# Kernel optimization log

Measured on AMD Instinct MI355X. Metric: run time of the kernel, lower is better.

## Reference

```python
import jax, jax.numpy as jnp
import numpy as np

IN_DIM, OUT_DIM, NUM, K = 128, 128, 5, 3
SIZE = IN_DIM * OUT_DIM  # number of spline activations
BATCH = 1024


def extend_grid(grid, k):
    # pykan: pad grid by k uniform steps on each side -> (size, num+1+2k)
    h = (grid[:, -1:] - grid[:, :1]) / (grid.shape[1] - 1)
    for _ in range(k):
        grid = jnp.concatenate([grid[:, :1] - h, grid, grid[:, -1:] + h], axis=1)
    return grid


def b_batch(x, grid, k):
    # Cox-de-Boor recursion, unrolled over fixed order k.
    # x: (size, batch), grid: (size, P) already extended. Returns (size, P-1-k, batch).
    x = x[:, None, :]        # (size, 1, batch)
    g = grid[:, :, None]     # (size, P, 1)
    B = ((x >= g[:, :-1]) & (x < g[:, 1:])).astype(x.dtype)  # order 0
    for p in range(1, k + 1):
        B = (x - g[:, :-(p + 1)]) / (g[:, p:-1] - g[:, :-(p + 1)]) * B[:, :-1] \
          + (g[:, p + 1:] - x) / (g[:, p + 1:] - g[:, 1:-p]) * B[:, 1:]
    return B


def setup_inputs() -> dict:
    key = jax.random.key(0)
    k1, k2 = jax.random.split(key)
    x = jax.random.normal(k1, (BATCH, IN_DIM), dtype=jnp.float32)
    # grid: identical uniform rows, as in torch.einsum('i,j->ij', ones(size), linspace)
    grid = jnp.tile(jnp.linspace(-1.0, 1.0, NUM + 1, dtype=jnp.float32)[None, :], (SIZE, 1))
    # coef: (size, num+k) spline coefficients (stand-in for curve2coef init)
    coef = jax.random.normal(k2, (SIZE, NUM + K), dtype=jnp.float32) * 0.1
    scale_base = jnp.ones((SIZE,), jnp.float32)
    scale_sp = jnp.ones((SIZE,), jnp.float32)
    mask = jnp.ones((SIZE,), jnp.float32)
    return {"x": x, "grid": grid, "coef": coef,
            "scale_base": scale_base, "scale_sp": scale_sp, "mask": mask}


def reference(x, grid, coef, scale_base, scale_sp, mask):
    batch = x.shape[0]
    # fan out x over out_dim: einsum('ij,k->ikj').reshape(batch,size).T -> (size, batch)
    xe = jnp.broadcast_to(x[:, None, :], (batch, OUT_DIM, IN_DIM)).reshape(batch, SIZE).T
    preacts = xe.T.reshape(batch, OUT_DIM, IN_DIM)
    base = jax.nn.silu(xe).T                                   # (batch, size)
    B = b_batch(xe, extend_grid(grid, K), K)                   # (size, num+k, batch)
    spline = jnp.einsum('ij,ijk->ik', coef, B).T               # (batch, size)
    postspline = spline.reshape(batch, OUT_DIM, IN_DIM)
    y = mask[None, :] * (scale_base[None, :] * base + scale_sp[None, :] * spline)
    postacts = y.reshape(batch, OUT_DIM, IN_DIM)
    y_out = postacts.sum(axis=2)                               # (batch, out_dim)
    return y_out, preacts, postacts, postspline
```

## Files before the change

### kernel.cpp

```cpp
#include <hip/hip_runtime.h>


#define IN_DIM  128
#define OUT_DIM 128
#define NUMG    5
#define KORD    3
#define NB      8
#define SIZE    (IN_DIM * OUT_DIM)
#define BATCH   1024
#define G       8
#define JB      8
#define NBG     (BATCH / G)
#define NJO     (OUT_DIM / JB)

__global__ __launch_bounds__(256) void kan_fused(
    const float* __restrict__ x,
    const float* __restrict__ grid,
    const float* __restrict__ coef,
    const float* __restrict__ scale_base,
    const float* __restrict__ scale_sp,
    const float* __restrict__ mask,
    float* __restrict__ out)
{
    __shared__ float sBT[G][NB][IN_DIM];
    __shared__ float sSilu[G][IN_DIM];
    __shared__ float sXv[G][IN_DIM];

    const int tid = threadIdx.x;
    const int bg  = blockIdx.x >> 4;
    const int jo  = blockIdx.x & (NJO - 1);

    const int lane = tid & 63;
    const int w    = tid >> 6;
    const int il   = lane & 31;
    const int jh   = lane >> 5;
    const int i4   = il << 2;
    const int j    = jo * JB + w * 2 + jh;

    float4 cfq[8];
    {
        const float4* cp = (const float4*)coef;
        #pragma unroll
        for (int q = 0; q < 8; ++q)
            cfq[q] = cp[(size_t)j * 256 + il * 8 + q];
    }
    const int sS = j * IN_DIM + i4;
    const float4 mkv = *(const float4*)&mask[sS];
    const float4 sbv = *(const float4*)&scale_base[sS];
    const float4 ssv = *(const float4*)&scale_sp[sS];

    {
        const int i  = tid & 127;
        const int r0 = tid >> 7;

        float gr[NUMG + 1];
        #pragma unroll
        for (int rr = 0; rr <= NUMG; ++rr) gr[rr] = grid[i * (NUMG + 1) + rr];

        const float h = (gr[NUMG] - gr[0]) * (1.0f / NUMG);
        float t[NUMG + 1 + 2 * KORD];
        t[2] = gr[0] - h; t[1] = t[2] - h; t[0] = t[1] - h;
        #pragma unroll
        for (int rr = 0; rr <= NUMG; ++rr) t[KORD + rr] = gr[rr];
        t[9] = gr[NUMG] + h; t[10] = t[9] + h; t[11] = t[10] + h;

        float rcp1[11], rcp2[10], rcp3[9];
        #pragma unroll
        for (int m = 0; m < 11; ++m) rcp1[m] = 1.0f / (t[m + 1] - t[m]);
        #pragma unroll
        for (int m = 0; m < 10; ++m) rcp2[m] = 1.0f / (t[m + 2] - t[m]);
        #pragma unroll
        for (int m = 0; m < 9;  ++m) rcp3[m] = 1.0f / (t[m + 3] - t[m]);

        #pragma unroll
        for (int it = 0; it < 4; ++it) {
            const int r = it * 2 + r0;
            const float xv = x[(bg * G + r) * IN_DIM + i];

            float B[NUMG + 2 * KORD];
            #pragma unroll
            for (int m = 0; m < NUMG + 2 * KORD; ++m)
                B[m] = (xv >= t[m] && xv < t[m + 1]) ? 1.0f : 0.0f;
            #pragma unroll
            for (int m = 0; m < 10; ++m)
                B[m] = (xv - t[m]) * rcp1[m] * B[m]
                     + (t[m + 2] - xv) * rcp1[m + 1] * B[m + 1];
            #pragma unroll
            for (int m = 0; m < 9; ++m)
                B[m] = (xv - t[m]) * rcp2[m] * B[m]
                     + (t[m + 3] - xv) * rcp2[m + 1] * B[m + 1];
            #pragma unroll
            for (int m = 0; m < 8; ++m)
                B[m] = (xv - t[m]) * rcp3[m] * B[m]
                     + (t[m + 4] - xv) * rcp3[m + 1] * B[m + 1];

            #pragma unroll
            for (int m = 0; m < NB; ++m) sBT[r][m][i] = B[m];
            sSilu[r][i] = xv / (1.0f + __expf(-xv));
            sXv[r][i]   = xv;
        }
    }
    __syncthreads();

    float cfs[4][NB];
    #pragma unroll
    for (int k = 0; k < 4; ++k) {
        const float4 lo = cfq[2 * k], hi = cfq[2 * k + 1];
        cfs[k][0] = lo.x; cfs[k][1] = lo.y; cfs[k][2] = lo.z; cfs[k][3] = lo.w;
        cfs[k][4] = hi.x; cfs[k][5] = hi.y; cfs[k][6] = hi.z; cfs[k][7] = hi.w;
    }
    const float mkA[4] = {mkv.x, mkv.y, mkv.z, mkv.w};
    const float sbA[4] = {sbv.x, sbv.y, sbv.z, sbv.w};
    const float ssA[4] = {ssv.x, ssv.y, ssv.z, ssv.w};

    float* out_y   = out;
    float* out_pre = out + BATCH * OUT_DIM;
    float* out_act = out_pre + (size_t)BATCH * SIZE;
    float* out_spl = out_act + (size_t)BATCH * SIZE;

    float py[G];

    #pragma unroll
    for (int r = 0; r < G; ++r) {
        float4 bas[NB];
        #pragma unroll
        for (int m = 0; m < NB; ++m)
            bas[m] = *(const float4*)&sBT[r][m][i4];

        float sp0 = cfs[0][0] * bas[0].x;
        float sp1 = cfs[1][0] * bas[0].y;
        float sp2 = cfs[2][0] * bas[0].z;
        float sp3 = cfs[3][0] * bas[0].w;
        #pragma unroll
        for (int m = 1; m < NB; ++m) {
            const float4 b4 = bas[m];
            sp0 = fmaf(cfs[0][m], b4.x, sp0);
            sp1 = fmaf(cfs[1][m], b4.y, sp1);
            sp2 = fmaf(cfs[2][m], b4.z, sp2);
            sp3 = fmaf(cfs[3][m], b4.w, sp3);
        }

        const float4 slv = *(const float4*)&sSilu[r][i4];
        const float4 pxv = *(const float4*)&sXv[r][i4];
        const float spA[4] = {sp0, sp1, sp2, sp3};
        const float slA[4] = {slv.x, slv.y, slv.z, slv.w};

        float y[4];
        #pragma unroll
        for (int k = 0; k < 4; ++k)
            y[k] = mkA[k] * (sbA[k] * slA[k] + ssA[k] * spA[k]);

        const int b_r = bg * G + r;
        const size_t e = (size_t)b_r * SIZE + (size_t)sS;
        *(float4*)&out_pre[e] = pxv;
        *(float4*)&out_act[e] = make_float4(y[0], y[1], y[2], y[3]);
        *(float4*)&out_spl[e] = make_float4(spA[0], spA[1], spA[2], spA[3]);

        py[r] = (y[0] + y[1]) + (y[2] + y[3]);
    }

    #pragma unroll
    for (int off = 16; off > 0; off >>= 1) {
        #pragma unroll
        for (int r = 0; r < G; ++r)
            py[r] += __shfl_down(py[r], off, 32);
    }
    if (il == 0) {
        #pragma unroll
        for (int r = 0; r < G; ++r)
            out_y[(bg * G + r) * OUT_DIM + j] = py[r];
    }
}

extern "C" void kernel_launch(void* const* d_in, const int* in_sizes, int n_in,
                              void* d_out, int out_size, void* d_ws, size_t ws_size,
                              hipStream_t stream)
{
    hipLaunchKernelGGL(kan_fused, dim3(NJO * NBG), dim3(256), 0, stream,
                       (const float*)d_in[0], (const float*)d_in[1],
                       (const float*)d_in[2], (const float*)d_in[3],
                       (const float*)d_in[4], (const float*)d_in[5],
                       (float*)d_out);
}
```

Baseline: 209.9 us.

## Split basis evaluation into a precompute kernel and a streaming output kernel

Adds a first kernel that evaluates the B-spline basis, SiLU and x once per (batch, input) pair and writes them to workspace. A second kernel reads those rows from global memory and streams the three large output tensors, with 16 batch rows per block. This removes the redundant basis recomputation the fused kernel did for every out_dim tile. It costs an extra launch, a workspace round trip, and sync-free global reads that replace the shared-memory reads. The fused kernel is kept as a fallback when no workspace is available.

```diff
diff --git a/kernel.cpp b/kernel.cpp
--- a/kernel.cpp
+++ b/kernel.cpp
@@ -12,6 +12,175 @@
 #define JB      8
 #define NBG     (BATCH / G)
 #define NJO     (OUT_DIM / JB)
+#define WSROW   (10 * IN_DIM)
+#define RCHUNK  16
+
+__device__ __forceinline__ void basis_row(const float* __restrict__ grid,
+                                          int i, float xv, float* __restrict__ B,
+                                          float& silu)
+{
+    float gr[NUMG + 1];
+    #pragma unroll
+    for (int rr = 0; rr <= NUMG; ++rr) gr[rr] = grid[i * (NUMG + 1) + rr];
+
+    const float h = (gr[NUMG] - gr[0]) * (1.0f / NUMG);
+    float t[NUMG + 1 + 2 * KORD];
+    t[2] = gr[0] - h; t[1] = t[2] - h; t[0] = t[1] - h;
+    #pragma unroll
+    for (int rr = 0; rr <= NUMG; ++rr) t[KORD + rr] = gr[rr];
+    t[9] = gr[NUMG] + h; t[10] = t[9] + h; t[11] = t[10] + h;
+
+    float rcp1[11], rcp2[10], rcp3[9];
+    #pragma unroll
+    for (int m = 0; m < 11; ++m) rcp1[m] = 1.0f / (t[m + 1] - t[m]);
+    #pragma unroll
+    for (int m = 0; m < 10; ++m) rcp2[m] = 1.0f / (t[m + 2] - t[m]);
+    #pragma unroll
+    for (int m = 0; m < 9;  ++m) rcp3[m] = 1.0f / (t[m + 3] - t[m]);
+
+    float Bt[NUMG + 2 * KORD];
+    #pragma unroll
+    for (int m = 0; m < NUMG + 2 * KORD; ++m)
+        Bt[m] = (xv >= t[m] && xv < t[m + 1]) ? 1.0f : 0.0f;
+    #pragma unroll
+    for (int m = 0; m < 10; ++m)
+        Bt[m] = (xv - t[m]) * rcp1[m] * Bt[m]
+              + (t[m + 2] - xv) * rcp1[m + 1] * Bt[m + 1];
+    #pragma unroll
+    for (int m = 0; m < 9; ++m)
+        Bt[m] = (xv - t[m]) * rcp2[m] * Bt[m]
+              + (t[m + 3] - xv) * rcp2[m + 1] * Bt[m + 1];
+    #pragma unroll
+    for (int m = 0; m < 8; ++m)
+        Bt[m] = (xv - t[m]) * rcp3[m] * Bt[m]
+              + (t[m + 4] - xv) * rcp3[m + 1] * Bt[m + 1];
+
+    #pragma unroll
+    for (int m = 0; m < NB; ++m) B[m] = Bt[m];
+    silu = xv / (1.0f + __expf(-xv));
+}
+
+__global__ __launch_bounds__(256) void kan_basis(
+    const float* __restrict__ x,
+    const float* __restrict__ grid,
+    float* __restrict__ ws)
+{
+    const int idx = blockIdx.x * 256 + threadIdx.x;
+    const int b = idx >> 7;
+    const int i = idx & 127;
+    const float xv = x[b * IN_DIM + i];
+
+    float B[NB], silu;
+    basis_row(grid, i, xv, B, silu);
+
+    float* wp = ws + (size_t)b * WSROW;
+    #pragma unroll
+    for (int m = 0; m < NB; ++m) wp[m * IN_DIM + i] = B[m];
+    wp[8 * IN_DIM + i] = silu;
+    wp[9 * IN_DIM + i] = xv;
+}
+
+__global__ __launch_bounds__(256) void kan_stream(
+    const float* __restrict__ ws,
+    const float* __restrict__ coef,
+    const float* __restrict__ scale_base,
+    const float* __restrict__ scale_sp,
+    const float* __restrict__ mask,
+    float* __restrict__ out)
+{
+    const int tid  = threadIdx.x;
+    const int lane = tid & 63;
+    const int w    = tid >> 6;
+    const int il   = lane & 31;
+    const int jh   = lane >> 5;
+    const int i4   = il << 2;
+
+    const int jo = blockIdx.x & (NJO - 1);
+    const int bc = blockIdx.x >> 4;
+    const int j  = jo * JB + w * 2 + jh;
+
+    float4 cfq[8];
+    {
+        const float4* cp = (const float4*)coef;
+        #pragma unroll
+        for (int q = 0; q < 8; ++q)
+            cfq[q] = cp[(size_t)j * 256 + il * 8 + q];
+    }
+    const int sS = j * IN_DIM + i4;
+    const float4 mkv = *(const float4*)&mask[sS];
+    const float4 sbv = *(const float4*)&scale_base[sS];
+    const float4 ssv = *(const float4*)&scale_sp[sS];
+
+    float cfs[4][NB];
+    #pragma unroll
+    for (int k = 0; k < 4; ++k) {
+        const float4 lo = cfq[2 * k], hi = cfq[2 * k + 1];
+        cfs[k][0] = lo.x; cfs[k][1] = lo.y; cfs[k][2] = lo.z; cfs[k][3] = lo.w;
+        cfs[k][4] = hi.x; cfs[k][5] = hi.y; cfs[k][6] = hi.z; cfs[k][7] = hi.w;
+    }
+    const float mkA[4] = {mkv.x, mkv.y, mkv.z, mkv.w};
+    const float sbA[4] = {sbv.x, sbv.y, sbv.z, sbv.w};
+    const float ssA[4] = {ssv.x, ssv.y, ssv.z, ssv.w};
+
+    float* out_y   = out;
+    float* out_pre = out + BATCH * OUT_DIM;
+    float* out_act = out_pre + (size_t)BATCH * SIZE;
+    float* out_spl = out_act + (size_t)BATCH * SIZE;
+
+    float py[RCHUNK];
+
+    #pragma unroll
+    for (int r = 0; r < RCHUNK; ++r) {
+        const int b_r = bc * RCHUNK + r;
+        const float* wp = ws + (size_t)b_r * WSROW;
+
+        float4 bas[NB];
+        #pragma unroll
+        for (int m = 0; m < NB; ++m)
+            bas[m] = *(const float4*)&wp[m * IN_DIM + i4];
+        const float4 slv = *(const float4*)&wp[8 * IN_DIM + i4];
+        const float4 pxv = *(const float4*)&wp[9 * IN_DIM + i4];
+
+        float sp0 = cfs[0][0] * bas[0].x;
+        float sp1 = cfs[1][0] * bas[0].y;
+        float sp2 = cfs[2][0] * bas[0].z;
+        float sp3 = cfs[3][0] * bas[0].w;
+        #pragma unroll
+        for (int m = 1; m < NB; ++m) {
+            const float4 b4 = bas[m];
+            sp0 = fmaf(cfs[0][m], b4.x, sp0);
+            sp1 = fmaf(cfs[1][m], b4.y, sp1);
+            sp2 = fmaf(cfs[2][m], b4.z, sp2);
+            sp3 = fmaf(cfs[3][m], b4.w, sp3);
+        }
+
+        const float spA[4] = {sp0, sp1, sp2, sp3};
+        const float slA[4] = {slv.x, slv.y, slv.z, slv.w};
+        float y[4];
+        #pragma unroll
+        for (int k = 0; k < 4; ++k)
+            y[k] = mkA[k] * (sbA[k] * slA[k] + ssA[k] * spA[k]);
+
+        const size_t e = (size_t)b_r * SIZE + (size_t)sS;
+        *(float4*)&out_pre[e] = pxv;
+        *(float4*)&out_act[e] = make_float4(y[0], y[1], y[2], y[3]);
+        *(float4*)&out_spl[e] = make_float4(spA[0], spA[1], spA[2], spA[3]);
+
+        py[r] = (y[0] + y[1]) + (y[2] + y[3]);
+    }
+
+    #pragma unroll
+    for (int off = 16; off > 0; off >>= 1) {
+        #pragma unroll
+        for (int r = 0; r < RCHUNK; ++r)
+            py[r] += __shfl_down(py[r], off, 32);
+    }
+    if (il == 0) {
+        #pragma unroll
+        for (int r = 0; r < RCHUNK; ++r)
+            out_y[(bc * RCHUNK + r) * OUT_DIM + j] = py[r];
+    }
+}
 
 __global__ __launch_bounds__(256) void kan_fused(
     const float* __restrict__ x,
@@ -52,51 +221,15 @@
     {
         const int i  = tid & 127;
         const int r0 = tid >> 7;
-
-        float gr[NUMG + 1];
-        #pragma unroll
-        for (int rr = 0; rr <= NUMG; ++rr) gr[rr] = grid[i * (NUMG + 1) + rr];
-
-        const float h = (gr[NUMG] - gr[0]) * (1.0f / NUMG);
-        float t[NUMG + 1 + 2 * KORD];
-        t[2] = gr[0] - h; t[1] = t[2] - h; t[0] = t[1] - h;
-        #pragma unroll
-        for (int rr = 0; rr <= NUMG; ++rr) t[KORD + rr] = gr[rr];
-        t[9] = gr[NUMG] + h; t[10] = t[9] + h; t[11] = t[10] + h;
-
-        float rcp1[11], rcp2[10], rcp3[9];
-        #pragma unroll
-        for (int m = 0; m < 11; ++m) rcp1[m] = 1.0f / (t[m + 1] - t[m]);
-        #pragma unroll
-        for (int m = 0; m < 10; ++m) rcp2[m] = 1.0f / (t[m + 2] - t[m]);
-        #pragma unroll
-        for (int m = 0; m < 9;  ++m) rcp3[m] = 1.0f / (t[m + 3] - t[m]);
-
         #pragma unroll
         for (int it = 0; it < 4; ++it) {
             const int r = it * 2 + r0;
             const float xv = x[(bg * G + r) * IN_DIM + i];
-
-            float B[NUMG + 2 * KORD];
-            #pragma unroll
-            for (int m = 0; m < NUMG + 2 * KORD; ++m)
-                B[m] = (xv >= t[m] && xv < t[m + 1]) ? 1.0f : 0.0f;
-            #pragma unroll
-            for (int m = 0; m < 10; ++m)
-                B[m] = (xv - t[m]) * rcp1[m] * B[m]
-                     + (t[m + 2] - xv) * rcp1[m + 1] * B[m + 1];
-            #pragma unroll
-            for (int m = 0; m < 9; ++m)
-                B[m] = (xv - t[m]) * rcp2[m] * B[m]
-                     + (t[m + 3] - xv) * rcp2[m + 1] * B[m + 1];
-            #pragma unroll
-            for (int m = 0; m < 8; ++m)
-                B[m] = (xv - t[m]) * rcp3[m] * B[m]
-                     + (t[m + 4] - xv) * rcp3[m + 1] * B[m + 1];
-
+            float B[NB], silu;
+            basis_row(grid, i, xv, B, silu);
             #pragma unroll
             for (int m = 0; m < NB; ++m) sBT[r][m][i] = B[m];
-            sSilu[r][i] = xv / (1.0f + __expf(-xv));
+            sSilu[r][i] = silu;
             sXv[r][i]   = xv;
         }
     }
@@ -119,7 +252,6 @@
     float* out_spl = out_act + (size_t)BATCH * SIZE;
 
     float py[G];
-
     #pragma unroll
     for (int r = 0; r < G; ++r) {
         float4 bas[NB];
@@ -144,7 +276,6 @@
         const float4 pxv = *(const float4*)&sXv[r][i4];
         const float spA[4] = {sp0, sp1, sp2, sp3};
         const float slA[4] = {slv.x, slv.y, slv.z, slv.w};
-
         float y[4];
         #pragma unroll
         for (int k = 0; k < 4; ++k)
@@ -176,9 +307,22 @@
                               void* d_out, int out_size, void* d_ws, size_t ws_size,
                               hipStream_t stream)
 {
-    hipLaunchKernelGGL(kan_fused, dim3(NJO * NBG), dim3(256), 0, stream,
-                       (const float*)d_in[0], (const float*)d_in[1],
-                       (const float*)d_in[2], (const float*)d_in[3],
-                       (const float*)d_in[4], (const float*)d_in[5],
-                       (float*)d_out);
-}
+    const size_t WS_NEED = (size_t)BATCH * WSROW * sizeof(float);
+    if (d_ws != nullptr && ws_size >= WS_NEED) {
+        hipLaunchKernelGGL(kan_basis, dim3(BATCH * IN_DIM / 256), dim3(256), 0,
+                           stream,
+                           (const float*)d_in[0], (const float*)d_in[1],
+                           (float*)d_ws);
+        hipLaunchKernelGGL(kan_stream, dim3((BATCH / RCHUNK) * NJO), dim3(256),
+                           0, stream,
+                           (const float*)d_ws, (const float*)d_in[2],
+                           (const float*)d_in[3], (const float*)d_in[4],
+                           (const float*)d_in[5], (float*)d_out);
+    } else {
+        hipLaunchKernelGGL(kan_fused, dim3(NJO * NBG), dim3(256), 0, stream,
+                           (const float*)d_in[0], (const float*)d_in[1],
+                           (const float*)d_in[2], (const float*)d_in[3],
+                           (const float*)d_in[4], (const float*)d_in[5],
+                           (float*)d_out);
+    }
+}
```

After: 219.0 us. +4.3%, slower.
